# Kernel optimization log

Measured on AMD Instinct MI355X. Metric: run time of the kernel, lower is better.

The kernel has to match this reference:

```python
import jax, jax.numpy as jnp
import numpy as np

NUM_EXPERTS = 7
TRUNK_DIM = 64
HIDDEN = 64   # max(48, trunk_dim)
NUM_DEPTH_CLASSES = 3
BATCH = 262144


def setup_inputs() -> dict:
    key = jax.random.key(0)
    ks = jax.random.split(key, 8)
    trunk_feat = jax.random.normal(ks[0], (BATCH, TRUNK_DIM), dtype=jnp.float32)
    size_idx = jax.random.randint(ks[1], (BATCH,), 0, NUM_EXPERTS, dtype=jnp.int64)
    # Stacked expert MLP params: Linear(64,64) -> ReLU -> Linear(64,64) -> ReLU -> Linear(64,3)
    s1 = 1.0 / np.sqrt(TRUNK_DIM)
    s2 = 1.0 / np.sqrt(HIDDEN)
    W1 = jax.random.uniform(ks[2], (NUM_EXPERTS, TRUNK_DIM, HIDDEN), jnp.float32, -s1, s1)
    b1 = jax.random.uniform(ks[3], (NUM_EXPERTS, HIDDEN), jnp.float32, -s1, s1)
    W2 = jax.random.uniform(ks[4], (NUM_EXPERTS, HIDDEN, HIDDEN), jnp.float32, -s2, s2)
    b2 = jax.random.uniform(ks[5], (NUM_EXPERTS, HIDDEN), jnp.float32, -s2, s2)
    W3 = jax.random.uniform(ks[6], (NUM_EXPERTS, HIDDEN, NUM_DEPTH_CLASSES), jnp.float32, -s2, s2)
    b3 = jax.random.uniform(ks[7], (NUM_EXPERTS, NUM_DEPTH_CLASSES), jnp.float32, -s2, s2)
    return {"trunk_feat": trunk_feat, "size_idx": size_idx,
            "W1": W1, "b1": b1, "W2": W2, "b2": b2, "W3": W3, "b3": b3}


def _expert_mlp(x, W1, b1, W2, b2, W3, b3):
    # 3-layer MLP of one expert (dropout = identity in eval mode)
    h = jax.nn.relu(x @ W1 + b1)
    h = jax.nn.relu(h @ W2 + b2)
    return h @ W3 + b3  # [B, num_depth_classes]


def reference(trunk_feat, size_idx, W1, b1, W2, b2, W3, b3):
    # Hard routing (route_logits): rows with size_idx == e go through expert e;
    # expressed as masked accumulate so it is jit-friendly (no data-dependent shapes).
    B = trunk_feat.shape[0]
    logits = jnp.zeros((B, NUM_DEPTH_CLASSES), dtype=trunk_feat.dtype)
    for e in range(NUM_EXPERTS):  # fixed, small expert count
        le = _expert_mlp(trunk_feat, W1[e], b1[e], W2[e], b2[e], W3[e], b3[e])
        mask = (size_idx == e)[:, None]
        logits = logits + jnp.where(mask, le, jnp.zeros_like(le))
    probs = jax.nn.softmax(logits, axis=1)
    return logits, probs
```

## Files before the change

kernel.cpp:

```cpp
#include <hip/hip_runtime.h>
#include <stdint.h>

#define NE    7
#define DD    64
#define NDC   3
#define BLOCK 256
#define ROWS  256
#define NFRAG 18

typedef __fp16   half8 __attribute__((ext_vector_type(8)));
typedef float    f32x4 __attribute__((ext_vector_type(4)));
typedef uint32_t u32x4 __attribute__((ext_vector_type(4)));
typedef uint32_t u32x2 __attribute__((ext_vector_type(2)));
typedef __fp16   h2_t  __attribute__((ext_vector_type(2)));

__device__ __forceinline__ uint32_t pkrtz(float a, float b) {
  h2_t h = __builtin_amdgcn_cvt_pkrtz(a, b);
  return __builtin_bit_cast(uint32_t, h);
}

__device__ __forceinline__ f32x4 mfma16(u32x4 a, u32x4 b, f32x4 c) {
  return __builtin_amdgcn_mfma_f32_16x16x32_f16(
      __builtin_bit_cast(half8, a), __builtin_bit_cast(half8, b), c, 0, 0, 0);
}

__device__ __forceinline__ u32x4 relu_pack(f32x4 lo, f32x4 hi) {
  u32x4 t = { pkrtz(fmaxf(lo[0],0.f), fmaxf(lo[1],0.f)),
              pkrtz(fmaxf(lo[2],0.f), fmaxf(lo[3],0.f)),
              pkrtz(fmaxf(hi[0],0.f), fmaxf(hi[1],0.f)),
              pkrtz(fmaxf(hi[2],0.f), fmaxf(hi[3],0.f)) };
  return t;
}

__global__ __launch_bounds__(BLOCK) void pack_w(
    const float* __restrict__ W1, const float* __restrict__ W2,
    const float* __restrict__ W3, uint32_t* __restrict__ ws) {
  const int e = blockIdx.x;
  const float* Wl0 = W1 + e*DD*DD;
  const float* Wl1 = W2 + e*DD*DD;
  const float* Wl2 = W3 + e*DD*NDC;
  for (int idx = threadIdx.x; idx < NFRAG*64; idx += BLOCK) {
    const int f = idx >> 6, l = idx & 63;
    int layer, fl;
    if (f < 8)       { layer = 0; fl = f; }
    else if (f < 16) { layer = 1; fl = f - 8; }
    else             { layer = 2; fl = f - 16; }
    const int nt = (layer < 2) ? (fl >> 1) : 0;
    const int ks = fl & 1;
    const int n  = nt*16 + (l & 15);
    const int g  = l >> 4;
    uint32_t dst[4];
    for (int d = 0; d < 4; ++d) {
      float v[2];
      for (int h = 0; h < 2; ++h) {
        const int kk = 16*(d>>1) + 4*g + 2*(d&1) + h;
        const int k  = 32*ks + kk;
        float val;
        if (layer == 0)      val = Wl0[k*DD + n];
        else if (layer == 1) val = Wl1[k*DD + n];
        else                 val = (n < NDC) ? Wl2[k*NDC + n] : 0.0f;
        v[h] = val;
      }
      dst[d] = pkrtz(v[0], v[1]);
    }
    uint32_t* p = ws + ((size_t)(e*NFRAG + f)*64 + l)*4;
    p[0]=dst[0]; p[1]=dst[1]; p[2]=dst[2]; p[3]=dst[3];
  }
}

__global__ __launch_bounds__(BLOCK, 3) void fused(
    const float* __restrict__ X, const int* __restrict__ S,
    const u32x4* __restrict__ wf,
    const float* __restrict__ b1, const float* __restrict__ b2,
    const float* __restrict__ b3,
    float* __restrict__ out, int B)
{
  __shared__ uint32_t pk[ROWS*32];
  __shared__ uint16_t srt[ROWS];
  __shared__ int wcnt[4][NE];
  __shared__ int woff[4][NE];
  __shared__ int cnt[NE];

  const int tid  = threadIdx.x;
  const int wv   = tid >> 6, lane = tid & 63;
  const int r15  = lane & 15, g = lane >> 4;
  const int base = blockIdx.x * ROWS;

  const int e_i = S[base + tid];
  unsigned long long mk[NE];
  #pragma unroll
  for (int e = 0; e < NE; ++e) mk[e] = __ballot(e_i == e);
  int myprefix = 0;
  #pragma unroll
  for (int e = 0; e < NE; ++e)
    if (e_i == e) myprefix = __popcll(mk[e] & ((1ull << lane) - 1ull));
  if (lane < NE) wcnt[wv][lane] = __popcll(mk[lane]);
  __syncthreads();

  if (tid == 0) {
    int acc = 0;
    for (int e = 0; e < NE; ++e) {
      const int s0 = acc;
      for (int w = 0; w < 4; ++w) { woff[w][e] = acc; acc += wcnt[w][e]; }
      cnt[e] = acc - s0;
    }
  }
  {
    const float4* Xb = (const float4*)(X + (size_t)base * DD);
    const int q     = lane & 15;
    const int rsub  = lane >> 4;
    const int ksq   = q >> 3, gq = q & 3, hq = (q >> 2) & 1;
    const int slotq = 4*ksq + gq;
    #pragma unroll
    for (int it = 0; it < 16; ++it) {
      const int r = wv*64 + it*4 + rsub;
      const float4 v = Xb[r*16 + q];
      u32x2 w2 = { pkrtz(v.x, v.y), pkrtz(v.z, v.w) };
      *(u32x2*)&pk[r*32 + ((slotq ^ (r & 7)) << 2) + hq*2] = w2;
    }
  }
  __syncthreads();

  srt[woff[wv][e_i] + myprefix] = (uint16_t)tid;
  __syncthreads();

  int pst[NE + 1];
  {
    int tp = 0;
    #pragma unroll
    for (int e = 0; e < NE; ++e) { pst[e] = tp; tp += (cnt[e] + 31) >> 5; }
    pst[NE] = tp;
  }

  for (int p = wv; p < pst[NE]; p += 4) {
    int e = 0;
    #pragma unroll
    for (int q2 = 1; q2 < NE; ++q2) if (p >= pst[q2]) e = q2;
    const int ch    = p - pst[e];
    const int m     = min(32, cnt[e] - ch*32);
    const int sbase = woff[0][e] + ch*32;

    const u32x4* wse = wf + (size_t)e*NFRAG*64;
    u32x4 af[NFRAG];
    #pragma unroll
    for (int f = 0; f < NFRAG; ++f) af[f] = wse[f*64 + lane];

    #pragma unroll 1
    for (int jt = 0; jt < 2; ++jt) {
      const int idx16 = min(jt*16 + r15, m - 1);
      const int lr    = srt[sbase + idx16];

      const u32x4 xf0 = *(const u32x4*)&pk[lr*32 + (((g    ) ^ (lr & 7)) << 2)];
      const u32x4 xf1 = *(const u32x4*)&pk[lr*32 + (((4 + g) ^ (lr & 7)) << 2)];

      f32x4 c[4];
      #pragma unroll
      for (int nt = 0; nt < 4; ++nt) {
        const float4 bv = *(const float4*)(b1 + e*DD + nt*16 + 4*g);
        f32x4 acc = { bv.x, bv.y, bv.z, bv.w };
        acc = mfma16(af[nt*2 + 0], xf0, acc);
        acc = mfma16(af[nt*2 + 1], xf1, acc);
        c[nt] = acc;
      }
      const u32x4 h0 = relu_pack(c[0], c[1]);
      const u32x4 h1 = relu_pack(c[2], c[3]);

      #pragma unroll
      for (int nt = 0; nt < 4; ++nt) {
        const float4 bv = *(const float4*)(b2 + e*DD + nt*16 + 4*g);
        f32x4 acc = { bv.x, bv.y, bv.z, bv.w };
        acc = mfma16(af[8 + nt*2 + 0], h0, acc);
        acc = mfma16(af[8 + nt*2 + 1], h1, acc);
        c[nt] = acc;
      }
      const u32x4 t0 = relu_pack(c[0], c[1]);
      const u32x4 t1 = relu_pack(c[2], c[3]);

      f32x4 acc = { b3[e*NDC + 0], b3[e*NDC + 1], b3[e*NDC + 2], 0.f };
      acc = mfma16(af[16], t0, acc);
      acc = mfma16(af[17], t1, acc);

      if (g == 0 && (jt*16 + r15) < m) {
        const int row = base + lr;
        const float l0 = acc[0], l1 = acc[1], l2 = acc[2];
        const float mx  = fmaxf(l0, fmaxf(l1, l2));
        const float p0  = __expf(l0 - mx);
        const float p1  = __expf(l1 - mx);
        const float p2  = __expf(l2 - mx);
        const float inv = 1.0f / (p0 + p1 + p2);
        float* o = out + (size_t)row*3;
        o[0] = l0; o[1] = l1; o[2] = l2;
        float* pr = out + (size_t)B*3 + (size_t)row*3;
        pr[0] = p0*inv; pr[1] = p1*inv; pr[2] = p2*inv;
      }
    }
  }
}

extern "C" void kernel_launch(void* const* d_in, const int* in_sizes, int n_in,
                              void* d_out, int out_size, void* d_ws, size_t ws_size,
                              hipStream_t stream)
{
  const float* X  = (const float*)d_in[0];
  const int*   S  = (const int*)d_in[1];
  const float* W1 = (const float*)d_in[2];
  const float* B1 = (const float*)d_in[3];
  const float* W2 = (const float*)d_in[4];
  const float* B2 = (const float*)d_in[5];
  const float* W3 = (const float*)d_in[6];
  const float* B3 = (const float*)d_in[7];
  float* out = (float*)d_out;
  uint32_t* ws = (uint32_t*)d_ws;

  const int B = in_sizes[0] / DD;

  pack_w<<<NE, BLOCK, 0, stream>>>(W1, W2, W3, ws);
  fused<<<B / ROWS, BLOCK, 0, stream>>>(X, S, (const u32x4*)ws,
                                        B1, B2, B3, out, B);
}
```

Before: 36.86 us.

## Load input tiles directly to LDS via global_load_lds with smaller row blocks

Result: no change. 37.60 us (+2.0%).

```diff
diff --git a/kernel.cpp b/kernel.cpp
--- a/kernel.cpp
+++ b/kernel.cpp
@@ -5,14 +5,16 @@
 #define DD    64
 #define NDC   3
 #define BLOCK 256
-#define ROWS  256
+#define ROWS  128
 #define NFRAG 18
 
 typedef __fp16   half8 __attribute__((ext_vector_type(8)));
 typedef float    f32x4 __attribute__((ext_vector_type(4)));
 typedef uint32_t u32x4 __attribute__((ext_vector_type(4)));
-typedef uint32_t u32x2 __attribute__((ext_vector_type(2)));
 typedef __fp16   h2_t  __attribute__((ext_vector_type(2)));
+
+typedef const void __attribute__((address_space(1))) gvoid_t;
+typedef void       __attribute__((address_space(3))) lvoid_t;
 
 __device__ __forceinline__ uint32_t pkrtz(float a, float b) {
   h2_t h = __builtin_amdgcn_cvt_pkrtz(a, b);
@@ -75,10 +77,10 @@
     const float* __restrict__ b3,
     float* __restrict__ out, int B)
 {
-  __shared__ uint32_t pk[ROWS*32];
+  __shared__ __align__(16) float pk[ROWS*DD];
   __shared__ uint16_t srt[ROWS];
-  __shared__ int wcnt[4][NE];
-  __shared__ int woff[4][NE];
+  __shared__ int wcnt[2][NE];
+  __shared__ int woff[2][NE];
   __shared__ int cnt[NE];
 
   const int tid  = threadIdx.x;
@@ -86,42 +88,44 @@
   const int r15  = lane & 15, g = lane >> 4;
   const int base = blockIdx.x * ROWS;
 
-  const int e_i = S[base + tid];
-  unsigned long long mk[NE];
-  #pragma unroll
-  for (int e = 0; e < NE; ++e) mk[e] = __ballot(e_i == e);
-  int myprefix = 0;
-  #pragma unroll
-  for (int e = 0; e < NE; ++e)
-    if (e_i == e) myprefix = __popcll(mk[e] & ((1ull << lane) - 1ull));
-  if (lane < NE) wcnt[wv][lane] = __popcll(mk[lane]);
+  int e_i = 0, myprefix = 0;
+  if (wv < 2) {
+    e_i = S[base + tid];
+    unsigned long long mk[NE];
+    #pragma unroll
+    for (int e = 0; e < NE; ++e) mk[e] = __ballot(e_i == e);
+    #pragma unroll
+    for (int e = 0; e < NE; ++e)
+      if (e_i == e) myprefix = __popcll(mk[e] & ((1ull << lane) - 1ull));
+    if (lane < NE) wcnt[wv][lane] = __popcll(mk[lane]);
+  }
+
+  {
+    const float* Xb = X + (size_t)base * DD;
+    #pragma unroll
+    for (int i = 0; i < 8; ++i) {
+      const int row  = wv*32 + i*4 + (lane >> 4);
+      const int slot = (lane & 15) ^ (row & 7);
+      const float* src = Xb + row*DD + slot*4;
+      lvoid_t* dst = (lvoid_t*)(pk + (wv*32 + i*4)*DD);
+      __builtin_amdgcn_global_load_lds((gvoid_t*)src, dst, 16, 0, 0);
+    }
+  }
   __syncthreads();
 
   if (tid == 0) {
     int acc = 0;
     for (int e = 0; e < NE; ++e) {
       const int s0 = acc;
-      for (int w = 0; w < 4; ++w) { woff[w][e] = acc; acc += wcnt[w][e]; }
+      for (int w = 0; w < 2; ++w) { woff[w][e] = acc; acc += wcnt[w][e]; }
       cnt[e] = acc - s0;
     }
   }
-  {
-    const float4* Xb = (const float4*)(X + (size_t)base * DD);
-    const int q     = lane & 15;
-    const int rsub  = lane >> 4;
-    const int ksq   = q >> 3, gq = q & 3, hq = (q >> 2) & 1;
-    const int slotq = 4*ksq + gq;
-    #pragma unroll
-    for (int it = 0; it < 16; ++it) {
-      const int r = wv*64 + it*4 + rsub;
-      const float4 v = Xb[r*16 + q];
-      u32x2 w2 = { pkrtz(v.x, v.y), pkrtz(v.z, v.w) };
-      *(u32x2*)&pk[r*32 + ((slotq ^ (r & 7)) << 2) + hq*2] = w2;
-    }
-  }
   __syncthreads();
 
-  srt[woff[wv][e_i] + myprefix] = (uint16_t)tid;
+  if (tid < ROWS) srt[woff[wv][e_i] + myprefix] = (uint16_t)tid;
+  asm volatile("s_waitcnt vmcnt(0)" ::: "memory");
+  __builtin_amdgcn_sched_barrier(0);
   __syncthreads();
 
   int pst[NE + 1];
@@ -147,19 +151,29 @@
 
     #pragma unroll 1
     for (int jt = 0; jt < 2; ++jt) {
+      if (jt && m <= 16) break;
       const int idx16 = min(jt*16 + r15, m - 1);
       const int lr    = srt[sbase + idx16];
 
-      const u32x4 xf0 = *(const u32x4*)&pk[lr*32 + (((g    ) ^ (lr & 7)) << 2)];
-      const u32x4 xf1 = *(const u32x4*)&pk[lr*32 + (((4 + g) ^ (lr & 7)) << 2)];
+      u32x4 xf[2];
+      #pragma unroll
+      for (int ks = 0; ks < 2; ++ks) {
+        const int s0 = (8*ks +     g) ^ (lr & 7);
+        const int s1 = (8*ks + 4 + g) ^ (lr & 7);
+        const f32x4 v0 = *(const f32x4*)&pk[lr*DD + s0*4];
+        const f32x4 v1 = *(const f32x4*)&pk[lr*DD + s1*4];
+        u32x4 t = { pkrtz(v0[0],v0[1]), pkrtz(v0[2],v0[3]),
+                    pkrtz(v1[0],v1[1]), pkrtz(v1[2],v1[3]) };
+        xf[ks] = t;
+      }
 
       f32x4 c[4];
       #pragma unroll
       for (int nt = 0; nt < 4; ++nt) {
         const float4 bv = *(const float4*)(b1 + e*DD + nt*16 + 4*g);
         f32x4 acc = { bv.x, bv.y, bv.z, bv.w };
-        acc = mfma16(af[nt*2 + 0], xf0, acc);
-        acc = mfma16(af[nt*2 + 1], xf1, acc);
+        acc = mfma16(af[nt*2 + 0], xf[0], acc);
+        acc = mfma16(af[nt*2 + 1], xf[1], acc);
         c[nt] = acc;
       }
       const u32x4 h0 = relu_pack(c[0], c[1]);
```
